# Optimization experiments

Measured on AMD Instinct MI355X. Metric: run time of the kernel, lower is better.

Reference implementation:

```python
import jax, jax.numpy as jnp
import numpy as np

B, S, D, DIM = 8, 4096, 1024, 512  # batch, src nodes, dst nodes, feature dim


def setup_inputs() -> dict:
    key = jax.random.key(0)
    k1, k2, k3, k4, k5 = jax.random.split(key, 5)
    scale = 1.0 / np.sqrt(DIM)
    return {
        "src_val": jax.random.normal(k1, (B, S, DIM), dtype=jnp.float32),
        "src_state": jax.random.normal(k2, (B, S), dtype=jnp.float32),
        "dst_val": jax.random.normal(k3, (B, D, DIM), dtype=jnp.float32),
        "W_route": jax.random.normal(k4, (DIM, DIM), dtype=jnp.float32) * scale,
        "W_val": jax.random.normal(k5, (DIM, DIM), dtype=jnp.float32) * scale,
    }


def reference(src_val, src_state, dst_val, W_route, W_val):
    # Pairwise route logits: bilinear bipartite attention, [B, S, D]
    inv_sqrt_d = 1.0 / jnp.sqrt(jnp.asarray(src_val.shape[-1], src_val.dtype))
    q = jnp.einsum("bsd,de->bse", src_val, W_route)
    logits = jnp.einsum("bse,bke->bsk", q, dst_val) * inv_sqrt_d
    # route compression: softmax over dst nodes (dim=-1)
    routes = jax.nn.softmax(logits, axis=-1)
    # projections
    projected_val = jnp.einsum("bsd,de->bse", src_val, W_val)  # [B, S, DIM]
    projected_state = src_state                                 # identity state proj, [B, S]
    sender_strength = jax.nn.softplus(src_state)                # [B, S]
    # weighted routing + accumulation
    weighted_routes = routes * sender_strength[..., None]       # [B, S, D]
    delta_state = jnp.einsum("bsk,bs->bk", weighted_routes, projected_state)   # [B, D]
    delta_val = jnp.einsum("bsk,bsd->bkd", weighted_routes, projected_val)     # [B, D, DIM]
    return delta_state, delta_val
```

## Files before the change

### kernel.cpp

```cpp
#include <hip/hip_runtime.h>
#include <hip/hip_fp16.h>

#define B_   8
#define S_   4096
#define DD_  1024
#define DIM_ 512
#define SCALE 0.044194173824159216f

typedef __bf16 bf16x8 __attribute__((ext_vector_type(8)));
typedef float  floatx4 __attribute__((ext_vector_type(4)));

__device__ inline unsigned short f2bf(float f) {
    union { float f; unsigned int u; } v; v.f = f;
    unsigned int r = v.u + 0x7fffu + ((v.u >> 16) & 1u);
    return (unsigned short)(r >> 16);
}
__device__ inline float bf2f(unsigned short h) {
    union { unsigned int u; float f; } v; v.u = ((unsigned int)h) << 16;
    return v.f;
}
__device__ inline uint4 cvt8(const float* __restrict__ g) {
    float4 f0 = *(const float4*)g;
    float4 f1 = *(const float4*)(g + 4);
    unsigned short tmp[8] = {f2bf(f0.x), f2bf(f0.y), f2bf(f0.z), f2bf(f0.w),
                             f2bf(f1.x), f2bf(f1.y), f2bf(f1.z), f2bf(f1.w)};
    return *(const uint4*)tmp;
}
__device__ inline void async16(unsigned short* lds, const unsigned short* g) {
    __builtin_amdgcn_global_load_lds(
        (const __attribute__((address_space(1))) void*)g,
        (__attribute__((address_space(3))) void*)lds, 16, 0, 0);
}

template <int N> __device__ inline void vwait() {
    if constexpr (N == 0)      asm volatile("s_waitcnt vmcnt(0)" ::: "memory");
    else if constexpr (N == 4) asm volatile("s_waitcnt vmcnt(4)" ::: "memory");
    else if constexpr (N == 6) asm volatile("s_waitcnt vmcnt(6)" ::: "memory");
    else                       asm volatile("s_waitcnt vmcnt(8)" ::: "memory");
}
#define SBAR   __builtin_amdgcn_s_barrier()
#define SCHED0 __builtin_amdgcn_sched_barrier(0)

__device__ inline void mainloop256(unsigned short* As, unsigned short* Bs,
                                   const unsigned short* __restrict__ Ap, size_t lda,
                                   const unsigned short* __restrict__ Bp, size_t ldb,
                                   int nk, floatx4 (&acc)[8][4]) {
    const int t = threadIdx.x, lane = t & 63, w = t >> 6;
    const int wm = w >> 2, wn = w & 3;
    const int fr = lane & 15;
    const int swz  = (((lane >> 4) ^ ((fr >> 1) & 3)) << 3);
    const int csrc = (((t & 3) ^ ((t >> 3) & 3)) << 3);

    const unsigned short* gA = Ap + (size_t)(t >> 2) * lda + csrc;
    const unsigned short* gB = Bp + (size_t)(t >> 2) * ldb + csrc;
    unsigned short* ldsA = As + w * 512;
    unsigned short* ldsB = Bs + w * 512;

    auto stgA = [&](int buf, int kt, int kh) {
        const unsigned short* g = gA + (size_t)kt * 64 + kh * 32;
        async16(ldsA + buf * 16384 + kh * 8192,        g);
        async16(ldsA + buf * 16384 + kh * 8192 + 4096, g + (size_t)128 * lda);
    };
    auto stgB = [&](int buf, int kt, int kh) {
        const unsigned short* g = gB + (size_t)kt * 64 + kh * 32;
        async16(ldsB + buf * 16384 + kh * 8192,        g);
        async16(ldsB + buf * 16384 + kh * 8192 + 4096, g + (size_t)128 * ldb);
    };

    stgA(0, 0, 0); stgB(0, 0, 0); stgA(0, 0, 1); stgB(0, 0, 1);
    stgA(1, 1, 0); stgB(1, 1, 0);
    vwait<8>();
    SCHED0;
    SBAR;

    const int arow = wm * 128 + fr, brow = wn * 64 + fr;
    bf16x8 a0[4], b0[4], a1[4], a2[4], b2[4], a3[4];
#pragma unroll
    for (int i = 0; i < 4; ++i) a0[i] = *(const bf16x8*)&As[(arow + i * 16) * 32 + swz];
#pragma unroll
    for (int j = 0; j < 4; ++j) b0[j] = *(const bf16x8*)&Bs[(brow + j * 16) * 32 + swz];

    for (int kt = 0; kt < nk; ++kt) {
        const int cur = kt & 1, base = cur * 16384;
        const bool sA = kt + 1 < nk, sB = kt + 2 < nk;
        if (sA) stgA(cur ^ 1, kt + 1, 1);
        SCHED0;
        __builtin_amdgcn_s_setprio(1);
#pragma unroll
        for (int i = 0; i < 4; ++i)
            a1[i] = *(const bf16x8*)&As[base + (arow + 64 + i * 16) * 32 + swz];
#pragma unroll
        for (int i = 0; i < 4; ++i)
#pragma unroll
            for (int j = 0; j < 4; ++j)
                acc[i][j] = __builtin_amdgcn_mfma_f32_16x16x32_bf16(a0[i], b0[j], acc[i][j], 0, 0, 0);
        __builtin_amdgcn_s_setprio(0);
        if (sA) vwait<6>(); else vwait<0>();
        SBAR;
        if (sA) stgB(cur ^ 1, kt + 1, 1);
        SCHED0;
        __builtin_amdgcn_s_setprio(1);
#pragma unroll
        for (int i = 0; i < 4; ++i)
            a2[i] = *(const bf16x8*)&As[base + 8192 + (arow + i * 16) * 32 + swz];
#pragma unroll
        for (int j = 0; j < 4; ++j)
            b2[j] = *(const bf16x8*)&Bs[base + 8192 + (brow + j * 16) * 32 + swz];
#pragma unroll
        for (int i = 0; i < 4; ++i)
#pragma unroll
            for (int j = 0; j < 4; ++j)
                acc[4 + i][j] = __builtin_amdgcn_mfma_f32_16x16x32_bf16(a1[i], b0[j], acc[4 + i][j], 0, 0, 0);
        __builtin_amdgcn_s_setprio(0);
        SBAR;
        if (sB) stgA(cur, kt + 2, 0);
        SCHED0;
        __builtin_amdgcn_s_setprio(1);
#pragma unroll
        for (int i = 0; i < 4; ++i)
            a3[i] = *(const bf16x8*)&As[base + 8192 + (arow + 64 + i * 16) * 32 + swz];
#pragma unroll
        for (int i = 0; i < 4; ++i)
#pragma unroll
            for (int j = 0; j < 4; ++j)
                acc[i][j] = __builtin_amdgcn_mfma_f32_16x16x32_bf16(a2[i], b2[j], acc[i][j], 0, 0, 0);
        __builtin_amdgcn_s_setprio(0);
        if (sA) { if (sB) vwait<6>(); else vwait<4>(); }
        SBAR;
        if (sB) stgB(cur, kt + 2, 0);
        SCHED0;
        __builtin_amdgcn_s_setprio(1);
        if (sA) {
            const int nb = (cur ^ 1) * 16384;
#pragma unroll
            for (int i = 0; i < 4; ++i)
                a0[i] = *(const bf16x8*)&As[nb + (arow + i * 16) * 32 + swz];
#pragma unroll
            for (int j = 0; j < 4; ++j)
                b0[j] = *(const bf16x8*)&Bs[nb + (brow + j * 16) * 32 + swz];
        }
#pragma unroll
        for (int i = 0; i < 4; ++i)
#pragma unroll
            for (int j = 0; j < 4; ++j)
                acc[4 + i][j] = __builtin_amdgcn_mfma_f32_16x16x32_bf16(a3[i], b2[j], acc[4 + i][j], 0, 0, 0);
        __builtin_amdgcn_s_setprio(0);
        SBAR;
    }
}

#define ACC_INIT8                                           \
    floatx4 acc[8][4];                                      \
    _Pragma("unroll") for (int i = 0; i < 8; ++i)           \
        _Pragma("unroll") for (int j = 0; j < 4; ++j)       \
            acc[i][j] = (floatx4){0.f, 0.f, 0.f, 0.f};

template <int AF32, int BF32>
__device__ inline void mainloop(unsigned short* As, unsigned short* Bs,
                                const void* Ap, size_t lda,
                                const void* Bp, size_t ldb,
                                int kIters, floatx4 (&acc)[4][4]) {
    const int t = threadIdx.x, lane = t & 63, wave = t >> 6;
    const int rA = t >> 2;
    const int cA = ((t & 3) ^ ((t >> 3) & 3)) * 8;
    const int mrow = (wave >> 1) * 64, ncol = (wave & 1) * 64;
    const int fr = lane & 15, fk = (lane >> 4) * 8;
    const int swz = (((fk >> 3) ^ ((fr >> 1) & 3)) << 3);

    const unsigned short* gA16 = nullptr; const float* gA32 = nullptr;
    const unsigned short* gB16 = nullptr; const float* gB32 = nullptr;
    if (AF32) gA32 = (const float*)Ap + (size_t)rA * lda + cA;
    else      gA16 = (const unsigned short*)Ap + (size_t)rA * lda + cA;
    if (BF32) gB32 = (const float*)Bp + (size_t)rA * ldb + cA;
    else      gB16 = (const unsigned short*)Bp + (size_t)rA * ldb + cA;

    unsigned short* ldsA = As + wave * 512;
    unsigned short* ldsB = Bs + wave * 512;

    auto stage = [&](int buf) {
        const int o = buf * 4096;
        if (AF32) {
            *(uint4*)&As[o + t * 8]        = cvt8(gA32);
            *(uint4*)&As[o + 2048 + t * 8] = cvt8(gA32 + 64 * lda);
            gA32 += 32;
        } else {
            async16(ldsA + o,        gA16);
            async16(ldsA + o + 2048, gA16 + 64 * lda);
            gA16 += 32;
        }
        if (BF32) {
            *(uint4*)&Bs[o + t * 8]        = cvt8(gB32);
            *(uint4*)&Bs[o + 2048 + t * 8] = cvt8(gB32 + 64 * ldb);
            gB32 += 32;
        } else {
            async16(ldsB + o,        gB16);
            async16(ldsB + o + 2048, gB16 + 64 * ldb);
            gB16 += 32;
        }
    };

    stage(0);
    __syncthreads();
    for (int kt = 0; kt < kIters; ++kt) {
        if (kt + 1 < kIters) stage((kt + 1) & 1);
        const int cur = (kt & 1) * 4096;
        bf16x8 af[4], bfr[4];
#pragma unroll
        for (int i = 0; i < 4; ++i)
            af[i] = *(const bf16x8*)&As[cur + (mrow + i * 16 + fr) * 32 + swz];
#pragma unroll
        for (int j = 0; j < 4; ++j)
            bfr[j] = *(const bf16x8*)&Bs[cur + (ncol + j * 16 + fr) * 32 + swz];
#pragma unroll
        for (int i = 0; i < 4; ++i)
#pragma unroll
            for (int j = 0; j < 4; ++j)
                acc[i][j] = __builtin_amdgcn_mfma_f32_16x16x32_bf16(af[i], bfr[j],
                                                                    acc[i][j], 0, 0, 0);
        __syncthreads();
    }
}

#define EPILOGUE_COORDS                                     \
    const int lane = threadIdx.x & 63, wave = threadIdx.x >> 6; \
    const int mrow = (wave >> 1) * 64, ncol = (wave & 1) * 64;  \
    const int col = lane & 15, q = lane >> 4;

#define ACC_INIT                                            \
    floatx4 acc[4][4];                                      \
    _Pragma("unroll") for (int i = 0; i < 4; ++i)           \
        _Pragma("unroll") for (int j = 0; j < 4; ++j)       \
            acc[i][j] = (floatx4){0.f, 0.f, 0.f, 0.f};

__global__ __launch_bounds__(256) void k_prep(const float* __restrict__ src,
                                              unsigned short* __restrict__ srcb) {
    const size_t idx = ((size_t)blockIdx.x * 256 + threadIdx.x) * 8;
    *(uint4*)&srcb[idx] = cvt8(src + idx);
}

__global__ __launch_bounds__(256) void k_dstWr(const float* __restrict__ dst,
                                               const float* __restrict__ Wr,
                                               unsigned short* __restrict__ DW) {
    __shared__ unsigned short As[2 * 128 * 32];
    __shared__ unsigned short Bs[2 * 128 * 32];
    const int n0 = blockIdx.x * 128, m0 = blockIdx.y * 128;
    ACC_INIT
    mainloop<1, 1>(As, Bs, dst + (size_t)m0 * DIM_, DIM_,
                   Wr + (size_t)n0 * DIM_, DIM_, DIM_ / 32, acc);
    EPILOGUE_COORDS
#pragma unroll
    for (int i = 0; i < 4; ++i)
#pragma unroll
        for (int j = 0; j < 4; ++j)
#pragma unroll
            for (int r = 0; r < 4; ++r)
                DW[(size_t)(m0 + mrow + i * 16 + q * 4 + r) * DIM_ +
                   n0 + ncol + j * 16 + col] = f2bf(acc[i][j][r] * SCALE);
}

__global__ __launch_bounds__(512, 2) void k_logitsT(const unsigned short* __restrict__ DW,
                                                    const unsigned short* __restrict__ srcb,
                                                    unsigned short* __restrict__ LTb,
                                                    float* __restrict__ Lpart) {
    __shared__ __align__(16) unsigned short As[32768];
    __shared__ __align__(16) unsigned short Bs[32768];
    const int n = blockIdx.x;
    const int b = n & 7;
    const int rem = n >> 3;
    const int xs = rem >> 2;
    const int yd = rem & 3;
    const int n0 = xs * 256, m0 = yd * 256;
    ACC_INIT8
    mainloop256(As, Bs,
                DW + (size_t)b * DD_ * DIM_ + (size_t)m0 * DIM_, DIM_,
                srcb + (size_t)b * S_ * DIM_ + (size_t)n0 * DIM_, DIM_,
                DIM_ / 64, acc);
    const int t = threadIdx.x, lane = t & 63, w = t >> 6;
    const int wm = w >> 2, wn = w & 3;
    const int c16 = lane & 15, q = lane >> 4;
    const int row0 = m0 + wm * 128, col0 = n0 + wn * 64;
    unsigned short* LT = LTb + (size_t)b * DD_ * S_;
    float psum[4] = {0.f, 0.f, 0.f, 0.f};
#pragma unroll
    for (int i = 0; i < 8; ++i)
#pragma unroll
        for (int j = 0; j < 4; ++j)
#pragma unroll
            for (int r = 0; r < 4; ++r) {
                float e = __expf(acc[i][j][r]);
                LT[(size_t)(row0 + i * 16 + q * 4 + r) * S_ +
                   col0 + j * 16 + c16] = f2bf(e);
                psum[j] += e;
            }
    float* csum = (float*)As;
    const int slice = wm * 4 + q;
#pragma unroll
    for (int j = 0; j < 4; ++j)
        csum[slice * 256 + wn * 64 + j * 16 + c16] = psum[j];
    __syncthreads();
    if (t < 256) {
        float v = 0.f;
#pragma unroll
        for (int k = 0; k < 8; ++k) v += csum[k * 256 + t];
        Lpart[((size_t)b * 4 + yd) * S_ + n0 + t] = v;
    }
}

__global__ __launch_bounds__(256) void k_finalize(const float* __restrict__ state,
                                                  const float* __restrict__ Lpart,
                                                  float* __restrict__ scale) {
    const int i = blockIdx.x * 256 + threadIdx.x;
    const int b = i >> 12, s = i & (S_ - 1);
    float d = 0.f;
#pragma unroll
    for (int k = 0; k < 4; ++k) d += Lpart[((size_t)b * 4 + k) * S_ + s];
    const float st = state[i];
    const float sp = (st > 15.f) ? st : log1pf(__expf(st));
    scale[i] = sp / d;
}

__global__ __launch_bounds__(256) void k_srcT(const unsigned short* __restrict__ srcb,
                                              const float* __restrict__ scale,
                                              unsigned short* __restrict__ srcST) {
    __shared__ unsigned short Ts[64 * 65];
    const int s0 = blockIdx.x * 64, d0 = blockIdx.y * 64, b = blockIdx.z;
    const int t = threadIdx.x;
    {
        const int r = t >> 2, c0 = (t & 3) * 16;
        const unsigned short* g =
            srcb + (size_t)b * S_ * DIM_ + (size_t)(s0 + r) * DIM_ + d0 + c0;
        uint4 v0 = *(const uint4*)g;
        uint4 v1 = *(const uint4*)(g + 8);
        const unsigned short* e0 = (const unsigned short*)&v0;
        const unsigned short* e1 = (const unsigned short*)&v1;
        const float sc = scale[(size_t)b * S_ + s0 + r];
#pragma unroll
        for (int i = 0; i < 8; ++i) {
            Ts[r * 65 + c0 + i]     = f2bf(bf2f(e0[i]) * sc);
            Ts[r * 65 + c0 + 8 + i] = f2bf(bf2f(e1[i]) * sc);
        }
    }
    __syncthreads();
    {
        const int rr = t >> 2, c0 = (t & 3) * 16;
        unsigned short tmp[16];
#pragma unroll
        for (int j = 0; j < 16; ++j) tmp[j] = Ts[(c0 + j) * 65 + rr];
        unsigned short* o =
            srcST + (size_t)b * DIM_ * S_ + (size_t)(d0 + rr) * S_ + s0 + c0;
        *(uint4*)o = *(const uint4*)tmp;
        *(uint4*)(o + 8) = *(const uint4*)(tmp + 8);
    }
}

__global__ __launch_bounds__(256) void k_dstate(const unsigned short* __restrict__ LT,
                                                const float* __restrict__ state,
                                                const float* __restrict__ scale,
                                                float* __restrict__ out) {
    const int b = blockIdx.y;
    const int dd = blockIdx.x * 4 + (threadIdx.x >> 6);
    const int lane = threadIdx.x & 63;
    const unsigned short* row = LT + (size_t)b * DD_ * S_ + (size_t)dd * S_;
    const float* st = state + (size_t)b * S_;
    const float* sc = scale + (size_t)b * S_;

    float acc = 0.f;
#pragma unroll
    for (int it = 0; it < S_ / 512; ++it) {
        const int s = it * 512 + lane * 8;
        uint4 v = *(const uint4*)(row + s);
        const unsigned short* e = (const unsigned short*)&v;
        float4 f0 = *(const float4*)(st + s);
        float4 f1 = *(const float4*)(st + s + 4);
        float4 c0 = *(const float4*)(sc + s);
        float4 c1 = *(const float4*)(sc + s + 4);
        acc += bf2f(e[0]) * f0.x * c0.x + bf2f(e[1]) * f0.y * c0.y +
               bf2f(e[2]) * f0.z * c0.z + bf2f(e[3]) * f0.w * c0.w +
               bf2f(e[4]) * f1.x * c1.x + bf2f(e[5]) * f1.y * c1.y +
               bf2f(e[6]) * f1.z * c1.z + bf2f(e[7]) * f1.w * c1.w;
    }
#pragma unroll
    for (int off = 32; off; off >>= 1) acc += __shfl_down(acc, off);
    if (lane == 0) out[(size_t)b * DD_ + dd] = acc;
}

__global__ __launch_bounds__(512, 2) void k_dU(const unsigned short* __restrict__ LTb,
                                               const unsigned short* __restrict__ srcST,
                                               __half* __restrict__ Pp) {
    __shared__ __align__(16) unsigned short As[32768];
    __shared__ __align__(16) unsigned short Bs[32768];
    const int n = blockIdx.x;
    const int qn = n >> 3;
    const int tile = qn & 7, zhi = qn >> 3;
    const int z = (n & 7) + 8 * zhi;
    const int b = z >> 2, ks = z & 3;
    const int xe = tile >> 2;
    const int yd = tile & 3;
    const int n0 = xe * 256, m0 = yd * 256;
    ACC_INIT8
    mainloop256(As, Bs,
                LTb + (size_t)b * DD_ * S_ + (size_t)m0 * S_ + ks * 1024, S_,
                srcST + (size_t)b * DIM_ * S_ + (size_t)n0 * S_ + ks * 1024, S_,
                1024 / 64, acc);
    const int t = threadIdx.x, lane = t & 63, w = t >> 6;
    const int wm = w >> 2, wn = w & 3;
    const int c16 = lane & 15, q = lane >> 4;
    const int row0 = m0 + wm * 128, col0 = n0 + wn * 64;
    __half* O = Pp + (size_t)ks * B_ * DD_ * DIM_ + (size_t)b * DD_ * DIM_;
#pragma unroll
    for (int i = 0; i < 8; ++i)
#pragma unroll
        for (int j = 0; j < 4; ++j)
#pragma unroll
            for (int r = 0; r < 4; ++r)
                O[(size_t)(row0 + i * 16 + q * 4 + r) * DIM_ +
                  col0 + j * 16 + c16] = __float2half(acc[i][j][r]);
}

__global__ __launch_bounds__(256) void k_reduceU(const __half* __restrict__ Pp,
                                                 unsigned short* __restrict__ U,
                                                 const float* __restrict__ Wv,
                                                 unsigned short* __restrict__ WvT) {
    __shared__ float Ts[64 * 68];
    const int t = threadIdx.x;
    if (blockIdx.x < 2048) {
        const size_t idx = ((size_t)blockIdx.x * 256 + t) * 8;
        const size_t n = (size_t)B_ * DD_ * DIM_;
        float o[8] = {0.f, 0.f, 0.f, 0.f, 0.f, 0.f, 0.f, 0.f};
#pragma unroll
        for (int ks = 0; ks < 4; ++ks) {
            uint4 v = *(const uint4*)(Pp + (size_t)ks * n + idx);
            const __half* h = (const __half*)&v;
#pragma unroll
            for (int j = 0; j < 8; ++j) o[j] += __half2float(h[j]);
        }
        unsigned short tmp[8];
#pragma unroll
        for (int j = 0; j < 8; ++j) tmp[j] = f2bf(o[j]);
        *(uint4*)&U[idx] = *(const uint4*)tmp;
        return;
    }
    const int n2 = blockIdx.x - 2048;
    const int d0 = (n2 & 7) * 64, e0 = (n2 >> 3) * 64;
    {
        const int r = t >> 2, c0 = (t & 3) * 16;
        const float* g = Wv + (size_t)(d0 + r) * DIM_ + e0 + c0;
#pragma unroll
        for (int i = 0; i < 4; ++i)
            *(float4*)&Ts[r * 68 + c0 + i * 4] = *(const float4*)(g + i * 4);
    }
    __syncthreads();
    {
        const int rr = t >> 2, c0 = (t & 3) * 16;
        unsigned short tmp[16];
#pragma unroll
        for (int j = 0; j < 16; ++j) tmp[j] = f2bf(Ts[(c0 + j) * 68 + rr]);
        unsigned short* o = WvT + (size_t)(e0 + rr) * DIM_ + d0 + c0;
        *(uint4*)o = *(const uint4*)tmp;
        *(uint4*)(o + 8) = *(const uint4*)(tmp + 8);
    }
}

__global__ __launch_bounds__(256) void k_dvalW(const unsigned short* __restrict__ U,
                                               const unsigned short* __restrict__ WvT,
                                               float* __restrict__ d_val) {
    __shared__ unsigned short As[2 * 128 * 32];
    __shared__ unsigned short Bs[2 * 128 * 32];
    const int n0 = blockIdx.x * 128, m0 = blockIdx.y * 128;
    ACC_INIT
    mainloop<0, 0>(As, Bs, U + (size_t)m0 * DIM_, DIM_,
                   WvT + (size_t)n0 * DIM_, DIM_, DIM_ / 32, acc);
    EPILOGUE_COORDS
#pragma unroll
    for (int i = 0; i < 4; ++i)
#pragma unroll
        for (int j = 0; j < 4; ++j)
#pragma unroll
            for (int r = 0; r < 4; ++r)
                d_val[(size_t)(m0 + mrow + i * 16 + q * 4 + r) * DIM_ +
                      n0 + ncol + j * 16 + col] = acc[i][j][r];
}

extern "C" void kernel_launch(void* const* d_in, const int* in_sizes, int n_in,
                              void* d_out, int out_size, void* d_ws, size_t ws_size,
                              hipStream_t stream) {
    const float* src   = (const float*)d_in[0];
    const float* state = (const float*)d_in[1];
    const float* dst   = (const float*)d_in[2];
    const float* Wr    = (const float*)d_in[3];
    const float* Wv    = (const float*)d_in[4];

    unsigned short* srcb = (unsigned short*)d_ws;
    __half* Pp = (__half*)d_ws;
    unsigned short* LT = srcb + (size_t)B_ * S_ * DIM_;
    unsigned short* U  = LT;
    unsigned short* WvT = U + (size_t)B_ * DD_ * DIM_;
    unsigned short* C = LT + (size_t)B_ * DD_ * S_;
    unsigned short* DW = C;
    float* Lpart = (float*)(DW + (size_t)B_ * DD_ * DIM_);
    unsigned short* srcST = C;

    float* d_state = (float*)d_out;
    float* d_val   = (float*)d_out + B_ * DD_;
    float* scale   = d_val;

    k_prep<<<dim3(8192), 256, 0, stream>>>(src, srcb);
    k_dstWr<<<dim3(DIM_ / 128, (B_ * DD_) / 128), 256, 0, stream>>>(dst, Wr, DW);
    k_logitsT<<<dim3(512), 512, 0, stream>>>(DW, srcb, LT, Lpart);
    k_finalize<<<dim3((B_ * S_) / 256), 256, 0, stream>>>(state, Lpart, scale);
    k_dstate<<<dim3(DD_ / 4, B_), 256, 0, stream>>>(LT, state, scale, d_state);
    k_srcT<<<dim3(S_ / 64, DIM_ / 64, B_), 256, 0, stream>>>(srcb, scale, srcST);
    k_dU<<<dim3(256), 512, 0, stream>>>(LT, srcST, Pp);
    k_reduceU<<<dim3(2048 + 64), 256, 0, stream>>>(Pp, U, Wv, WvT);
    k_dvalW<<<dim3(DIM_ / 128, (B_ * DD_) / 128), 256, 0, stream>>>(U, WvT, d_val);
}
```

Baseline: 272.3 us.

## Merge independent kernels and fuse split-K reduction into final GEMM staging

```diff
diff --git a/kernel.cpp b/kernel.cpp
--- a/kernel.cpp
+++ b/kernel.cpp
@@ -6,6 +6,7 @@
 #define DD_  1024
 #define DIM_ 512
 #define SCALE 0.044194173824159216f
+#define PPN  ((size_t)B_ * DD_ * DIM_)
 
 typedef __bf16 bf16x8 __attribute__((ext_vector_type(8)));
 typedef float  floatx4 __attribute__((ext_vector_type(4)));
@@ -232,18 +233,21 @@
         _Pragma("unroll") for (int j = 0; j < 4; ++j)       \
             acc[i][j] = (floatx4){0.f, 0.f, 0.f, 0.f};
 
-__global__ __launch_bounds__(256) void k_prep(const float* __restrict__ src,
-                                              unsigned short* __restrict__ srcb) {
-    const size_t idx = ((size_t)blockIdx.x * 256 + threadIdx.x) * 8;
-    *(uint4*)&srcb[idx] = cvt8(src + idx);
-}
-
-__global__ __launch_bounds__(256) void k_dstWr(const float* __restrict__ dst,
+__global__ __launch_bounds__(256) void k_front(const float* __restrict__ src,
+                                               unsigned short* __restrict__ srcb,
+                                               const float* __restrict__ dst,
                                                const float* __restrict__ Wr,
                                                unsigned short* __restrict__ DW) {
     __shared__ unsigned short As[2 * 128 * 32];
     __shared__ unsigned short Bs[2 * 128 * 32];
-    const int n0 = blockIdx.x * 128, m0 = blockIdx.y * 128;
+    const int bx = blockIdx.x;
+    if (bx < 8192) {
+        const size_t idx = ((size_t)bx * 256 + threadIdx.x) * 8;
+        *(uint4*)&srcb[idx] = cvt8(src + idx);
+        return;
+    }
+    const int i2 = bx - 8192;
+    const int n0 = (i2 & 3) * 128, m0 = (i2 >> 2) * 128;
     ACC_INIT
     mainloop<1, 1>(As, Bs, dst + (size_t)m0 * DIM_, DIM_,
                    Wr + (size_t)n0 * DIM_, DIM_, DIM_ / 32, acc);
@@ -308,7 +312,8 @@
 
 __global__ __launch_bounds__(256) void k_finalize(const float* __restrict__ state,
                                                   const float* __restrict__ Lpart,
-                                                  float* __restrict__ scale) {
+                                                  float* __restrict__ scale,
+                                                  float* __restrict__ w) {
     const int i = blockIdx.x * 256 + threadIdx.x;
     const int b = i >> 12, s = i & (S_ - 1);
     float d = 0.f;
@@ -316,15 +321,46 @@
     for (int k = 0; k < 4; ++k) d += Lpart[((size_t)b * 4 + k) * S_ + s];
     const float st = state[i];
     const float sp = (st > 15.f) ? st : log1pf(__expf(st));
-    scale[i] = sp / d;
-}
-
-__global__ __launch_bounds__(256) void k_srcT(const unsigned short* __restrict__ srcb,
-                                              const float* __restrict__ scale,
-                                              unsigned short* __restrict__ srcST) {
+    const float sc = sp / d;
+    scale[i] = sc;
+    w[i] = sc * st;
+}
+
+__global__ __launch_bounds__(256) void k_mid(const unsigned short* __restrict__ LTb,
+                                             const float* __restrict__ w,
+                                             const unsigned short* __restrict__ srcb,
+                                             const float* __restrict__ scale,
+                                             unsigned short* __restrict__ srcST,
+                                             float* __restrict__ out) {
     __shared__ unsigned short Ts[64 * 65];
-    const int s0 = blockIdx.x * 64, d0 = blockIdx.y * 64, b = blockIdx.z;
+    const int bx = blockIdx.x;
     const int t = threadIdx.x;
+    if (bx < 2048) {
+        const int b = bx >> 8;
+        const int dd = (bx & 255) * 4 + (t >> 6);
+        const int lane = t & 63;
+        const unsigned short* row = LTb + (size_t)b * DD_ * S_ + (size_t)dd * S_;
+        const float* wp = w + (size_t)b * S_;
+        float acc = 0.f;
+#pragma unroll
+        for (int it = 0; it < S_ / 512; ++it) {
+            const int s = it * 512 + lane * 8;
+            uint4 v = *(const uint4*)(row + s);
+            const unsigned short* e = (const unsigned short*)&v;
+            float4 w0 = *(const float4*)(wp + s);
+            float4 w1 = *(const float4*)(wp + s + 4);
+            acc += bf2f(e[0]) * w0.x + bf2f(e[1]) * w0.y +
+                   bf2f(e[2]) * w0.z + bf2f(e[3]) * w0.w +
+                   bf2f(e[4]) * w1.x + bf2f(e[5]) * w1.y +
+                   bf2f(e[6]) * w1.z + bf2f(e[7]) * w1.w;
+        }
+#pragma unroll
+        for (int off = 32; off; off >>= 1) acc += __shfl_down(acc, off);
+        if (lane == 0) out[(size_t)b * DD_ + dd] = acc;
+        return;
+    }
+    const int i2 = bx - 2048;
+    const int s0 = (i2 & 63) * 64, d0 = ((i2 >> 6) & 7) * 64, b = i2 >> 9;
     {
         const int r = t >> 2, c0 = (t & 3) * 16;
         const unsigned short* g =
@@ -351,37 +387,6 @@
         *(uint4*)o = *(const uint4*)tmp;
         *(uint4*)(o + 8) = *(const uint4*)(tmp + 8);
     }
-}
-
-__global__ __launch_bounds__(256) void k_dstate(const unsigned short* __restrict__ LT,
-                                                const float* __restrict__ state,
-                                                const float* __restrict__ scale,
-                                                float* __restrict__ out) {
-    const int b = blockIdx.y;
-    const int dd = blockIdx.x * 4 + (threadIdx.x >> 6);
-    const int lane = threadIdx.x & 63;
-    const unsigned short* row = LT + (size_t)b * DD_ * S_ + (size_t)dd * S_;
-    const float* st = state + (size_t)b * S_;
-    const float* sc = scale + (size_t)b * S_;
-
-    float acc = 0.f;
-#pragma unroll
-    for (int it = 0; it < S_ / 512; ++it) {
-        const int s = it * 512 + lane * 8;
-        uint4 v = *(const uint4*)(row + s);
-        const unsigned short* e = (const unsigned short*)&v;
-        float4 f0 = *(const float4*)(st + s);
-        float4 f1 = *(const float4*)(st + s + 4);
-        float4 c0 = *(const float4*)(sc + s);
-        float4 c1 = *(const float4*)(sc + s + 4);
-        acc += bf2f(e[0]) * f0.x * c0.x + bf2f(e[1]) * f0.y * c0.y +
-               bf2f(e[2]) * f0.z * c0.z + bf2f(e[3]) * f0.w * c0.w +
-               bf2f(e[4]) * f1.x * c1.x + bf2f(e[5]) * f1.y * c1.y +
-               bf2f(e[6]) * f1.z * c1.z + bf2f(e[7]) * f1.w * c1.w;
-    }
-#pragma unroll
-    for (int off = 32; off; off >>= 1) acc += __shfl_down(acc, off);
-    if (lane == 0) out[(size_t)b * DD_ + dd] = acc;
 }
 
 __global__ __launch_bounds__(512, 2) void k_dU(const unsigned short* __restrict__ LTb,
@@ -406,7 +411,7 @@
     const int wm = w >> 2, wn = w & 3;
     const int c16 = lane & 15, q = lane >> 4;
     const int row0 = m0 + wm * 128, col0 = n0 + wn * 64;
-    __half* O = Pp + (size_t)ks * B_ * DD_ * DIM_ + (size_t)b * DD_ * DIM_;
+    __half* O = Pp + (size_t)ks * PPN + (size_t)b * DD_ * DIM_;
 #pragma unroll
     for (int i = 0; i < 8; ++i)
 #pragma unroll
@@ -417,60 +422,74 @@
                   col0 + j * 16 + c16] = __float2half(acc[i][j][r]);
 }
 
-__global__ __launch_bounds__(256) void k_reduceU(const __half* __restrict__ Pp,
-                                                 unsigned short* __restrict__ U,
-                                                 const float* __restrict__ Wv,
-                                                 unsigned short* __restrict__ WvT) {
-    __shared__ float Ts[64 * 68];
-    const int t = threadIdx.x;
-    if (blockIdx.x < 2048) {
-        const size_t idx = ((size_t)blockIdx.x * 256 + t) * 8;
-        const size_t n = (size_t)B_ * DD_ * DIM_;
-        float o[8] = {0.f, 0.f, 0.f, 0.f, 0.f, 0.f, 0.f, 0.f};
-#pragma unroll
-        for (int ks = 0; ks < 4; ++ks) {
-            uint4 v = *(const uint4*)(Pp + (size_t)ks * n + idx);
-            const __half* h = (const __half*)&v;
-#pragma unroll
-            for (int j = 0; j < 8; ++j) o[j] += __half2float(h[j]);
-        }
-        unsigned short tmp[8];
-#pragma unroll
-        for (int j = 0; j < 8; ++j) tmp[j] = f2bf(o[j]);
-        *(uint4*)&U[idx] = *(const uint4*)tmp;
-        return;
-    }
-    const int n2 = blockIdx.x - 2048;
-    const int d0 = (n2 & 7) * 64, e0 = (n2 >> 3) * 64;
-    {
-        const int r = t >> 2, c0 = (t & 3) * 16;
-        const float* g = Wv + (size_t)(d0 + r) * DIM_ + e0 + c0;
-#pragma unroll
-        for (int i = 0; i < 4; ++i)
-            *(float4*)&Ts[r * 68 + c0 + i * 4] = *(const float4*)(g + i * 4);
-    }
-    __syncthreads();
-    {
-        const int rr = t >> 2, c0 = (t & 3) * 16;
-        unsigned short tmp[16];
-#pragma unroll
-        for (int j = 0; j < 16; ++j) tmp[j] = f2bf(Ts[(c0 + j) * 68 + rr]);
-        unsigned short* o = WvT + (size_t)(e0 + rr) * DIM_ + d0 + c0;
-        *(uint4*)o = *(const uint4*)tmp;
-        *(uint4*)(o + 8) = *(const uint4*)(tmp + 8);
-    }
-}
-
-__global__ __launch_bounds__(256) void k_dvalW(const unsigned short* __restrict__ U,
-                                               const unsigned short* __restrict__ WvT,
-                                               float* __restrict__ d_val) {
+__global__ __launch_bounds__(256) void k_dvalW2(const __half* __restrict__ Pp,
+                                                const float* __restrict__ Wv,
+                                                float* __restrict__ d_val) {
     __shared__ unsigned short As[2 * 128 * 32];
     __shared__ unsigned short Bs[2 * 128 * 32];
     const int n0 = blockIdx.x * 128, m0 = blockIdx.y * 128;
+    const int t = threadIdx.x;
+    const int rA = t >> 2, cA = ((t & 3) ^ ((t >> 3) & 3)) * 8;
+    const __half* gA = Pp + (size_t)(m0 + rA) * DIM_ + cA;
+    const int d0 = (t >> 4) * 2;
+    const int ecol = t & 15;
+
     ACC_INIT
-    mainloop<0, 0>(As, Bs, U + (size_t)m0 * DIM_, DIM_,
-                   WvT + (size_t)n0 * DIM_, DIM_, DIM_ / 32, acc);
-    EPILOGUE_COORDS
+    auto stageA8 = [&](unsigned short* dst, const __half* g) {
+        float o[8] = {0.f, 0.f, 0.f, 0.f, 0.f, 0.f, 0.f, 0.f};
+#pragma unroll
+        for (int ksl = 0; ksl < 4; ++ksl) {
+            uint4 v = *(const uint4*)(g + (size_t)ksl * PPN);
+            const __half* h = (const __half*)&v;
+#pragma unroll
+            for (int j = 0; j < 8; ++j) o[j] += __half2float(h[j]);
+        }
+        unsigned short tmp[8];
+#pragma unroll
+        for (int j = 0; j < 8; ++j) tmp[j] = f2bf(o[j]);
+        *(uint4*)dst = *(const uint4*)tmp;
+    };
+    auto stage = [&](int buf, int kt) {
+        const int o = buf * 4096;
+        stageA8(&As[o + t * 8],        gA + kt * 32);
+        stageA8(&As[o + 2048 + t * 8], gA + kt * 32 + (size_t)64 * DIM_);
+        const float* wv = Wv + (size_t)(kt * 32 + d0) * DIM_ + n0 + ecol;
+#pragma unroll
+        for (int i = 0; i < 8; ++i) {
+            float v0 = wv[16 * i];
+            float v1 = wv[16 * i + DIM_];
+            unsigned int pk = (unsigned int)f2bf(v0) | ((unsigned int)f2bf(v1) << 16);
+            const int e = ecol + 16 * i;
+            const int phys = e * 32 + (((d0 >> 3) ^ ((e >> 1) & 3)) << 3) + (d0 & 7);
+            *(unsigned int*)&Bs[o + phys] = pk;
+        }
+    };
+
+    stage(0, 0);
+    __syncthreads();
+    const int lane = t & 63, wave = t >> 6;
+    const int mrow = (wave >> 1) * 64, ncol = (wave & 1) * 64;
+    const int fr = lane & 15, fk = (lane >> 4) * 8;
+    const int swz = (((fk >> 3) ^ ((fr >> 1) & 3)) << 3);
+    for (int kt = 0; kt < DIM_ / 32; ++kt) {
+        if (kt + 1 < DIM_ / 32) stage((kt + 1) & 1, kt + 1);
+        const int cur = (kt & 1) * 4096;
+        bf16x8 af[4], bfr[4];
+#pragma unroll
+        for (int i = 0; i < 4; ++i)
+            af[i] = *(const bf16x8*)&As[cur + (mrow + i * 16 + fr) * 32 + swz];
+#pragma unroll
+        for (int j = 0; j < 4; ++j)
+            bfr[j] = *(const bf16x8*)&Bs[cur + (ncol + j * 16 + fr) * 32 + swz];
+#pragma unroll
+        for (int i = 0; i < 4; ++i)
+#pragma unroll
+            for (int j = 0; j < 4; ++j)
+                acc[i][j] = __builtin_amdgcn_mfma_f32_16x16x32_bf16(af[i], bfr[j],
+                                                                    acc[i][j], 0, 0, 0);
+        __syncthreads();
+    }
+    const int col = lane & 15, q = lane >> 4;
 #pragma unroll
     for (int i = 0; i < 4; ++i)
 #pragma unroll
@@ -493,8 +512,6 @@
     unsigned short* srcb = (unsigned short*)d_ws;
     __half* Pp = (__half*)d_ws;
     unsigned short* LT = srcb + (size_t)B_ * S_ * DIM_;
-    unsigned short* U  = LT;
-    unsigned short* WvT = U + (size_t)B_ * DD_ * DIM_;
     unsigned short* C = LT + (size_t)B_ * DD_ * S_;
     unsigned short* DW = C;
     float* Lpart = (float*)(DW + (size_t)B_ * DD_ * DIM_);
@@ -503,14 +520,12 @@
     float* d_state = (float*)d_out;
     float* d_val   = (float*)d_out + B_ * DD_;
     float* scale   = d_val;
-
-    k_prep<<<dim3(8192), 256, 0, stream>>>(src, srcb);
-    k_dstWr<<<dim3(DIM_ / 128, (B_ * DD_) / 128), 256, 0, stream>>>(dst, Wr, DW);
+    float* w       = d_val + (size_t)B_ * S_;
+
+    k_front<<<dim3(8192 + 256), 256, 0, stream>>>(src, srcb, dst, Wr, DW);
     k_logitsT<<<dim3(512), 512, 0, stream>>>(DW, srcb, LT, Lpart);
-    k_finalize<<<dim3((B_ * S_) / 256), 256, 0, stream>>>(state, Lpart, scale);
-    k_dstate<<<dim3(DD_ / 4, B_), 256, 0, stream>>>(LT, state, scale, d_state);
-    k_srcT<<<dim3(S_ / 64, DIM_ / 64, B_), 256, 0, stream>>>(srcb, scale, srcST);
+    k_finalize<<<dim3((B_ * S_) / 256), 256, 0, stream>>>(state, Lpart, scale, w);
+    k_mid<<<dim3(2048 + 4096), 256, 0, stream>>>(LT, w, srcb, scale, srcST, d_state);
     k_dU<<<dim3(256), 512, 0, stream>>>(LT, srcST, Pp);
-    k_reduceU<<<dim3(2048 + 64), 256, 0, stream>>>(Pp, U, Wv, WvT);
-    k_dvalW<<<dim3(DIM_ / 128, (B_ * DD_) / 128), 256, 0, stream>>>(U, WvT, d_val);
-}
+    k_dvalW2<<<dim3(DIM_ / 128, (B_ * DD_) / 128), 256, 0, stream>>>(Pp, Wv, d_val);
+}
```

Result: slower. 291.5 us (+7.1%).
